# Performance work log

Measured on AMD Instinct MI355X. Metric: run time of the kernel, lower is better.

The kernel has to match this reference:

```python
import jax, jax.numpy as jnp
import numpy as np

B, N, C = 8, 1024, 768
H = 12
HD = C // H
R = 16  # LoRA rank
SCALE = HD ** -0.5


def setup_inputs() -> dict:
    key = jax.random.key(0)
    ks = jax.random.split(key, 13)
    s = C ** -0.5
    return {
        "x": jax.random.normal(ks[0], (B, N, C), jnp.float32),
        "Wq": jax.random.normal(ks[1], (C, C), jnp.float32) * s,
        "Wk": jax.random.normal(ks[2], (C, C), jnp.float32) * s,
        "Wv": jax.random.normal(ks[3], (C, C), jnp.float32) * s,
        "Wp": jax.random.normal(ks[4], (C, C), jnp.float32) * s,
        "bp": jax.random.normal(ks[5], (C,), jnp.float32) * 0.02,
        "la_q": jax.random.normal(ks[6], (C, R), jnp.float32) * s,
        "lb_q": jax.random.normal(ks[7], (R, C), jnp.float32) * (R ** -0.5),
        "la_k": jax.random.normal(ks[8], (C, R), jnp.float32) * s,
        "lb_k": jax.random.normal(ks[9], (R, C), jnp.float32) * (R ** -0.5),
        "la_v": jax.random.normal(ks[10], (C, R), jnp.float32) * s,
        "lb_v": jax.random.normal(ks[11], (R, C), jnp.float32) * (R ** -0.5),
        "block_weight": jax.random.uniform(ks[12], (3,), jnp.float32),
    }


def _split_heads(t):
    # [B, N, C] -> [B, H, N, HD]
    return t.reshape(B, N, H, HD).transpose(0, 2, 1, 3)


def reference(x, Wq, Wk, Wv, Wp, bp, la_q, lb_q, la_k, lb_k, la_v, lb_v, block_weight):
    # q/k/v projections (qkv_bias=False) + LoRA adapter injection (msa=[1,1,1])
    q = x @ Wq + block_weight[0] * ((x @ la_q) @ lb_q)
    k = x @ Wk + block_weight[1] * ((x @ la_k) @ lb_k)
    v = x @ Wv + block_weight[2] * ((x @ la_v) @ lb_v)

    qh = _split_heads(q)  # [B,H,N,HD]
    kh = _split_heads(k)
    vh = _split_heads(v)

    # full NxN scores, scale, softmax (attn_drop=0 -> identity)
    attn = jnp.einsum("bhnd,bhmd->bhnm", qh, kh) * SCALE
    attn = jax.nn.softmax(attn, axis=-1)
    out = jnp.einsum("bhnm,bhmd->bhnd", attn, vh)  # [B,H,N,HD]
    out = out.transpose(0, 2, 1, 3).reshape(B, N, C)

    # output projection (proj_drop=0 -> identity)
    return out @ Wp + bp
```

## Files before the change

### kernel.cpp

```cpp
#include <hip/hip_runtime.h>

#define BB 8
#define NN 1024
#define CC 768
#define HH 12
#define HD 64
#define RR 16
#define MM (BB * NN)
#define WSZ (CC * CC)
#define NT (NN / 64)

#define KSC 0.18033688011112042f

typedef short bf16x8 __attribute__((ext_vector_type(8)));
typedef short bf16x4 __attribute__((ext_vector_type(4)));
typedef float f32x4 __attribute__((ext_vector_type(4)));

__device__ __forceinline__ unsigned short f2bf(float f) {
    unsigned u = __builtin_bit_cast(unsigned, f);
    unsigned r = (u + 0x7FFFu + ((u >> 16) & 1u)) >> 16;
    return (unsigned short)r;
}
__device__ __forceinline__ float bf2f(unsigned short s) {
    return __builtin_bit_cast(float, ((unsigned)s) << 16);
}

__device__ __forceinline__ float fast_exp2(float x) {
#if __has_builtin(__builtin_amdgcn_exp2f)
    return __builtin_amdgcn_exp2f(x);
#else
    return exp2f(x);
#endif
}

__device__ __forceinline__ unsigned cvt_pk_bf16(float a, float b) {
    unsigned r;
    asm("v_cvt_pk_bf16_f32 %0, %1, %2" : "=v"(r) : "v"(a), "v"(b));
    return r;
}

__device__ __forceinline__ void gload16(const void* g, void* l) {
    __builtin_amdgcn_global_load_lds(
        (const __attribute__((address_space(1))) unsigned int*)g,
        (__attribute__((address_space(3))) unsigned int*)l, 16, 0, 0);
}

__global__ __launch_bounds__(256) void prep_w(
    const float* __restrict__ Wq, const float* __restrict__ Wk,
    const float* __restrict__ Wv, const float* __restrict__ Wp,
    const float* __restrict__ la_q, const float* __restrict__ lb_q,
    const float* __restrict__ la_k, const float* __restrict__ lb_k,
    const float* __restrict__ la_v, const float* __restrict__ lb_v,
    const float* __restrict__ bw, short* __restrict__ wt_hi,
    short* __restrict__ wt_lo) {
    __shared__ float laS[64][16];
    __shared__ float lbS[16][64];
    __shared__ float T[64][65];

    const int z = blockIdx.z;
    const int k0 = blockIdx.y * 64, n0 = blockIdx.x * 64;
    const int tid = threadIdx.x;

    const float* W = (z == 0) ? Wq : (z == 1) ? Wk : (z == 2) ? Wv : Wp;
    const float* la = (z == 0) ? la_q : (z == 1) ? la_k : la_v;
    const float* lb = (z == 0) ? lb_q : (z == 1) ? lb_k : lb_v;
    const float bwz = (z < 3) ? bw[z] : 0.f;

    if (z < 3) {
        #pragma unroll
        for (int e = 0; e < 4; ++e) {
            int idx = tid + 256 * e;
            laS[idx >> 4][idx & 15] = la[(size_t)(k0 + (idx >> 4)) * RR + (idx & 15)];
            lbS[idx >> 6][idx & 63] = lb[(size_t)(idx >> 6) * CC + n0 + (idx & 63)];
        }
    }
    __syncthreads();

    #pragma unroll
    for (int e = 0; e < 16; ++e) {
        int idx = tid + 256 * e;
        int row = idx >> 6, col = idx & 63;
        float v = W[(size_t)(k0 + row) * CC + n0 + col];
        if (z < 3) {
            float s = 0.f;
            #pragma unroll
            for (int r = 0; r < 16; ++r) s += laS[row][r] * lbS[r][col];
            v += bwz * s;
        }
        T[row][col] = v;
    }
    __syncthreads();

    short* oh = wt_hi + (size_t)z * WSZ;
    short* ol = wt_lo + (size_t)z * WSZ;
    #pragma unroll
    for (int e = 0; e < 16; ++e) {
        int idx = tid + 256 * e;
        int nrow = idx >> 6, kcol = idx & 63;
        float v = T[kcol][nrow];
        unsigned short hi = f2bf(v);
        unsigned short lo = f2bf(v - bf2f(hi));
        size_t off = (size_t)(n0 + nrow) * CC + k0 + kcol;
        oh[off] = (short)hi;
        ol[off] = (short)lo;
    }
}

__global__ __launch_bounds__(256) void prep_cvt(const float* __restrict__ src,
                                                short* __restrict__ hi, int n4) {
    int i = blockIdx.x * 256 + threadIdx.x;
    const int stride = gridDim.x * 256;
    for (; i < n4; i += stride) {
        f32x4 v = ((const f32x4*)src)[i];
        bf16x4 h;
        #pragma unroll
        for (int c = 0; c < 4; ++c) h[c] = (short)f2bf(v[c]);
        ((bf16x4*)hi)[i] = h;
    }
}

__device__ __forceinline__ void stage_plain(const short* __restrict__ gA,
                                            const short* __restrict__ gB,
                                            int rowA0, int rowB0, int kt,
                                            short* Lb, int tid) {
    const int fr = ((tid >> 6) << 4) | (tid & 15);
    const int kc = ((tid >> 4) & 3) * 8 + kt;
    const size_t ga0 = (size_t)(rowA0 + fr) * CC + kc;
    const size_t gb0 = (size_t)(rowB0 + fr) * CC + kc;
    short* d0 = Lb + tid * 8;
    short* d1 = Lb + (tid + 256) * 8;
    gload16(gA + ga0, d0);
    gload16(gA + ga0 + (size_t)64 * CC, d1);
    gload16(gB + gb0, d0 + 4096);
    gload16(gB + gb0 + (size_t)64 * CC, d1 + 4096);
}

__device__ __forceinline__ void gemm_core_plain(const short* __restrict__ gA,
                                                int rowA0,
                                                const short* __restrict__ gB,
                                                int rowB0, short (*L)[8192],
                                                f32x4 acc[4][4]) {
    const int tid = threadIdx.x, lane = tid & 63, w = tid >> 6;
    const int wm = w >> 1, wn = w & 1;
    stage_plain(gA, gB, rowA0, rowB0, 0, L[0], tid);
    __syncthreads();
    for (int ki = 0; ki < 24; ++ki) {
        if (ki < 23)
            stage_plain(gA, gB, rowA0, rowB0, (ki + 1) * 32, L[(ki + 1) & 1],
                        tid);
        const short* Lb = L[ki & 1];
        bf16x8 ah[4], bh[4];
        #pragma unroll
        for (int i = 0; i < 4; ++i)
            ah[i] = *(const bf16x8*)(Lb + (wm * 4 + i) * 512 + lane * 8);
        #pragma unroll
        for (int j = 0; j < 4; ++j)
            bh[j] = *(const bf16x8*)(Lb + 4096 + (wn * 4 + j) * 512 + lane * 8);
        #pragma unroll
        for (int i = 0; i < 4; ++i)
            #pragma unroll
            for (int j = 0; j < 4; ++j)
                acc[i][j] = __builtin_amdgcn_mfma_f32_16x16x32_bf16(
                    ah[i], bh[j], acc[i][j], 0, 0, 0);
        __syncthreads();
    }
}

__global__ __launch_bounds__(256, 4) void gemm_qkv(
    const short* __restrict__ xh, const short* __restrict__ wth,
    short* __restrict__ qb, short* __restrict__ kb, short* __restrict__ vtb) {
    __shared__ __align__(16) short L[2][8192];

    int flat = blockIdx.x + 6 * blockIdx.y + 384 * blockIdx.z;
    int swz = (flat & 7) * 144 + (flat >> 3);
    int z = swz / 384;
    int rem = swz - z * 384;
    int by = rem / 6, bx = rem - by * 6;
    const int m0 = by * 128, c0 = bx * 128;

    const short* wzh = wth + (size_t)z * WSZ;

    f32x4 acc[4][4];
    const f32x4 z4 = {0.f, 0.f, 0.f, 0.f};
    #pragma unroll
    for (int i = 0; i < 4; ++i)
        #pragma unroll
        for (int j = 0; j < 4; ++j) acc[i][j] = z4;

    const int lane = threadIdx.x & 63, w = threadIdx.x >> 6;
    const int wm = w >> 1, wn = w & 1, p = lane & 15, g = lane >> 4;

    if (z < 2) {
        gemm_core_plain(xh, m0, wzh, c0, L, acc);
        short* dst = (z == 0) ? qb : kb;
        const float scl = (z == 0) ? KSC : 1.0f;
        #pragma unroll
        for (int i = 0; i < 4; ++i) {
            #pragma unroll
            for (int r = 0; r < 4; ++r) {
                int m = m0 + wm * 64 + i * 16 + 4 * g + r;
                int b = m >> 10, n = m & 1023;
                #pragma unroll
                for (int j = 0; j < 4; ++j) {
                    int c = c0 + wn * 64 + j * 16 + p;
                    int h = c >> 6, d = c & 63;
                    dst[(((size_t)(b * HH + h)) * NN + n) * HD + d] =
                        (short)f2bf(acc[i][j][r] * scl);
                }
            }
        }
    } else {
        gemm_core_plain(wzh, c0, xh, m0, L, acc);
        #pragma unroll
        for (int i = 0; i < 4; ++i) {
            #pragma unroll
            for (int r = 0; r < 4; ++r) {
                int c = c0 + wm * 64 + i * 16 + 4 * g + r;
                int h = c >> 6, d = c & 63;
                #pragma unroll
                for (int j = 0; j < 4; ++j) {
                    int m = m0 + wn * 64 + j * 16 + p;
                    int b = m >> 10, n = m & 1023;
                    vtb[(((size_t)(b * HH + h)) * HD + d) * NN + n] =
                        (short)f2bf(acc[i][j][r]);
                }
            }
        }
    }
}

__device__ __forceinline__ void stage_kv(const short* __restrict__ kp,
                                         const short* __restrict__ vp, int j0,
                                         short* Kd, short* Vd, int tid) {
    const int pp = tid & 15;
    const int kc = ((tid >> 4) & 3) * 8 + ((tid >> 6) & 1) * 32;
    const int r0 = tid >> 7;
    gload16(kp + (size_t)(j0 + r0 * 16 + pp) * HD + kc, Kd + tid * 8);
    gload16(kp + (size_t)(j0 + (r0 + 2) * 16 + pp) * HD + kc, Kd + (tid + 256) * 8);
    gload16(vp + (size_t)(r0 * 16 + pp) * NN + j0 + kc, Vd + tid * 8);
    gload16(vp + (size_t)((r0 + 2) * 16 + pp) * NN + j0 + kc, Vd + (tid + 256) * 8);
}

__global__ __launch_bounds__(256, 4) void attn(const short* __restrict__ qb,
                                               const short* __restrict__ kb,
                                               const short* __restrict__ vtb,
                                               short* __restrict__ aoh,
                                               short* __restrict__ aol) {
    __shared__ __align__(16) short QP[4096];
    __shared__ __align__(16) short Kb[2][4096];
    __shared__ __align__(16) short Vb[2][4096];

    int flat = blockIdx.x + 16 * blockIdx.y;
    int swz = (flat & 7) * 192 + (flat >> 3);
    const int q0 = (swz & 15) * 64;
    const int bh = swz >> 4;

    const int tid = threadIdx.x, lane = tid & 63, w = tid >> 6;
    const int p = lane & 15, g = lane >> 4;
    const short* qp = qb + (size_t)bh * NN * HD;
    const short* kp = kb + (size_t)bh * NN * HD;
    const short* vp = vtb + (size_t)bh * NN * HD;

    {
        const int kc = ((tid >> 4) & 3) * 8 + ((tid >> 6) & 1) * 32;
        const int r0 = tid >> 7;
        gload16(qp + (size_t)(q0 + r0 * 16 + p) * HD + kc, QP + tid * 8);
        gload16(qp + (size_t)(q0 + (r0 + 2) * 16 + p) * HD + kc,
                QP + (tid + 256) * 8);
    }
    stage_kv(kp, vp, 0, Kb[0], Vb[0], tid);
    __syncthreads();

    bf16x8 bQ[2];
    bQ[0] = *(const bf16x8*)(QP + (w * 2 + 0) * 512 + lane * 8);
    bQ[1] = *(const bf16x8*)(QP + (w * 2 + 1) * 512 + lane * 8);

    float m_run = -1e30f, l_run = 0.f;
    f32x4 oacc[4];
    const f32x4 z4 = {0.f, 0.f, 0.f, 0.f};
    #pragma unroll
    for (int df = 0; df < 4; ++df) oacc[df] = z4;
    short* Pw = QP + w * 1024;

    for (int t = 0; t < NT; ++t) {
        if (t < NT - 1)
            stage_kv(kp, vp, (t + 1) * 64, Kb[(t + 1) & 1], Vb[(t + 1) & 1], tid);
        const short* Kc = Kb[t & 1];
        const short* Vc = Vb[t & 1];

        f32x4 sacc[4];
        #pragma unroll
        for (int jf = 0; jf < 4; ++jf) sacc[jf] = z4;
        #pragma unroll
        for (int ks = 0; ks < 2; ++ks) {
            #pragma unroll
            for (int jf = 0; jf < 4; ++jf) {
                bf16x8 aK =
                    *(const bf16x8*)(Kc + jf * 1024 + ks * 512 + lane * 8);
                sacc[jf] = __builtin_amdgcn_mfma_f32_16x16x32_bf16(
                    aK, bQ[ks], sacc[jf], 0, 0, 0);
            }
        }

        float tmax = sacc[0][0];
        #pragma unroll
        for (int jf = 0; jf < 4; ++jf)
            #pragma unroll
            for (int r = 0; r < 4; ++r) tmax = fmaxf(tmax, sacc[jf][r]);
        tmax = fmaxf(tmax, __shfl_xor(tmax, 16));
        tmax = fmaxf(tmax, __shfl_xor(tmax, 32));
        if (__any(tmax > m_run + 3.0f)) {
            const float mnew = fmaxf(m_run, tmax);
            const float fac = fast_exp2(m_run - mnew);
            m_run = mnew;
            l_run *= fac;
            #pragma unroll
            for (int r = 0; r < 4; ++r) {
                float fr = __shfl(fac, 4 * g + r, 16);
                #pragma unroll
                for (int df = 0; df < 4; ++df) oacc[df][r] *= fr;
            }
        }
        float lsum = 0.f;
        #pragma unroll
        for (int jf = 0; jf < 4; ++jf) {
            #pragma unroll
            for (int r = 0; r < 4; ++r) {
                float e = fast_exp2(sacc[jf][r] - m_run);
                sacc[jf][r] = e;
                lsum += e;
            }
        }
        lsum += __shfl_xor(lsum, 16);
        lsum += __shfl_xor(lsum, 32);
        l_run += lsum;

        #pragma unroll
        for (int jf = 0; jf < 4; ++jf) {
            uint2 wpk;
            wpk.x = cvt_pk_bf16(sacc[jf][0], sacc[jf][1]);
            wpk.y = cvt_pk_bf16(sacc[jf][2], sacc[jf][3]);
            *(uint2*)(Pw + (jf >> 1) * 512 +
                      (((jf & 1) * 2 + (g >> 1)) * 16 + p) * 8 + (g & 1) * 4) =
                wpk;
        }
        asm volatile("s_waitcnt lgkmcnt(0)" ::: "memory");
        __builtin_amdgcn_sched_barrier(0);

        #pragma unroll
        for (int ks = 0; ks < 2; ++ks) {
            bf16x8 aP = *(const bf16x8*)(Pw + ks * 512 + lane * 8);
            #pragma unroll
            for (int df = 0; df < 4; ++df) {
                bf16x8 bV =
                    *(const bf16x8*)(Vc + df * 1024 + ks * 512 + lane * 8);
                oacc[df] = __builtin_amdgcn_mfma_f32_16x16x32_bf16(
                    aP, bV, oacc[df], 0, 0, 0);
            }
        }
        __syncthreads();
    }

    const float inv = 1.f / l_run;
    const int b = bh / HH, h = bh % HH;
    #pragma unroll
    for (int r = 0; r < 4; ++r) {
        float ir = __shfl(inv, 4 * g + r, 16);
        int n = q0 + w * 16 + 4 * g + r;
        #pragma unroll
        for (int df = 0; df < 4; ++df) {
            float v = oacc[df][r] * ir;
            unsigned short hi = f2bf(v);
            unsigned short lo = f2bf(v - bf2f(hi));
            size_t off = ((size_t)(b * NN + n)) * CC + h * HD + df * 16 + p;
            aoh[off] = (short)hi;
            aol[off] = (short)lo;
        }
    }
}

__device__ __forceinline__ void stage_split(const short* __restrict__ gAh,
                                            const short* __restrict__ gAl,
                                            const short* __restrict__ gBh,
                                            const short* __restrict__ gBl,
                                            int rowA0, int rowB0, int kt,
                                            short* Lb, int tid) {
    const int fr = ((tid >> 6) << 4) | (tid & 15);
    const int kc = ((tid >> 4) & 3) * 8 + kt;
    const size_t ga0 = (size_t)(rowA0 + fr) * CC + kc;
    const size_t ga1 = ga0 + (size_t)64 * CC;
    const size_t gb0 = (size_t)(rowB0 + fr) * CC + kc;
    const size_t gb1 = gb0 + (size_t)64 * CC;
    short* d0 = Lb + tid * 8;
    short* d1 = Lb + (tid + 256) * 8;
    gload16(gAh + ga0, d0);
    gload16(gAh + ga1, d1);
    gload16(gAl + ga0, d0 + 4096);
    gload16(gAl + ga1, d1 + 4096);
    gload16(gBh + gb0, d0 + 8192);
    gload16(gBh + gb1, d1 + 8192);
    gload16(gBl + gb0, d0 + 12288);
    gload16(gBl + gb1, d1 + 12288);
}

__global__ __launch_bounds__(256, 3) void gemm_proj(
    const short* __restrict__ aoh, const short* __restrict__ aol,
    const short* __restrict__ wth, const short* __restrict__ wtl,
    const float* __restrict__ bp, float* __restrict__ out) {
    __shared__ __align__(16) short L[4 * 4096];

    int flat = blockIdx.x + 6 * blockIdx.y;
    int swz = (flat & 7) * 48 + (flat >> 3);
    int by = swz / 6, bx = swz - by * 6;
    const int m0 = by * 128, c0 = bx * 128;

    const short* wph = wth + (size_t)3 * WSZ;
    const short* wpl = wtl + (size_t)3 * WSZ;

    f32x4 acc[4][4];
    const f32x4 z4 = {0.f, 0.f, 0.f, 0.f};
    #pragma unroll
    for (int i = 0; i < 4; ++i)
        #pragma unroll
        for (int j = 0; j < 4; ++j) acc[i][j] = z4;

    const int tid = threadIdx.x, lane = tid & 63, w = tid >> 6;
    const int wm = w >> 1, wn = w & 1, p = lane & 15, g = lane >> 4;

    for (int kt = 0; kt < CC; kt += 32) {
        if (kt) __syncthreads();
        stage_split(aoh, aol, wph, wpl, m0, c0, kt, L, tid);
        __syncthreads();
        const int fb = lane * 8;
        bf16x8 ah[4], al[4], bh[4], bl[4];
        #pragma unroll
        for (int i = 0; i < 4; ++i) {
            ah[i] = *(const bf16x8*)(L + (wm * 4 + i) * 512 + fb);
            al[i] = *(const bf16x8*)(L + 4096 + (wm * 4 + i) * 512 + fb);
        }
        #pragma unroll
        for (int j = 0; j < 4; ++j) {
            bh[j] = *(const bf16x8*)(L + 8192 + (wn * 4 + j) * 512 + fb);
            bl[j] = *(const bf16x8*)(L + 12288 + (wn * 4 + j) * 512 + fb);
        }
        #pragma unroll
        for (int i = 0; i < 4; ++i) {
            #pragma unroll
            for (int j = 0; j < 4; ++j) {
                acc[i][j] = __builtin_amdgcn_mfma_f32_16x16x32_bf16(
                    ah[i], bh[j], acc[i][j], 0, 0, 0);
                acc[i][j] = __builtin_amdgcn_mfma_f32_16x16x32_bf16(
                    ah[i], bl[j], acc[i][j], 0, 0, 0);
                acc[i][j] = __builtin_amdgcn_mfma_f32_16x16x32_bf16(
                    al[i], bh[j], acc[i][j], 0, 0, 0);
            }
        }
    }

    float bpv[4];
    #pragma unroll
    for (int j = 0; j < 4; ++j) bpv[j] = bp[c0 + wn * 64 + j * 16 + p];

    #pragma unroll
    for (int i = 0; i < 4; ++i) {
        #pragma unroll
        for (int r = 0; r < 4; ++r) {
            int m = m0 + wm * 64 + i * 16 + 4 * g + r;
            #pragma unroll
            for (int j = 0; j < 4; ++j) {
                int c = c0 + wn * 64 + j * 16 + p;
                out[(size_t)m * CC + c] = acc[i][j][r] + bpv[j];
            }
        }
    }
}

extern "C" void kernel_launch(void* const* d_in, const int* in_sizes, int n_in,
                              void* d_out, int out_size, void* d_ws,
                              size_t ws_size, hipStream_t stream) {
    const float* x = (const float*)d_in[0];
    const float* Wq = (const float*)d_in[1];
    const float* Wk = (const float*)d_in[2];
    const float* Wv = (const float*)d_in[3];
    const float* Wp = (const float*)d_in[4];
    const float* bp = (const float*)d_in[5];
    const float* la_q = (const float*)d_in[6];
    const float* lb_q = (const float*)d_in[7];
    const float* la_k = (const float*)d_in[8];
    const float* lb_k = (const float*)d_in[9];
    const float* la_v = (const float*)d_in[10];
    const float* lb_v = (const float*)d_in[11];
    const float* bw = (const float*)d_in[12];
    float* out = (float*)d_out;

    short* ws = (short*)d_ws;
    short* wt_hi = ws;
    short* wt_lo = wt_hi + (size_t)4 * WSZ;
    short* x_hi = wt_lo + (size_t)4 * WSZ;
    short* qbuf = x_hi + (size_t)MM * CC;
    short* kbuf = qbuf + (size_t)MM * CC;
    short* vtbuf = kbuf + (size_t)MM * CC;
    short* aoh = vtbuf + (size_t)MM * CC;
    short* aol = aoh + (size_t)MM * CC;

    prep_w<<<dim3(CC / 64, CC / 64, 4), 256, 0, stream>>>(
        Wq, Wk, Wv, Wp, la_q, lb_q, la_k, lb_k, la_v, lb_v, bw, wt_hi, wt_lo);
    prep_cvt<<<2048, 256, 0, stream>>>(x, x_hi, MM * CC / 4);
    gemm_qkv<<<dim3(CC / 128, MM / 128, 3), 256, 0, stream>>>(
        x_hi, wt_hi, qbuf, kbuf, vtbuf);
    attn<<<dim3(NN / 64, BB * HH), 256, 0, stream>>>(qbuf, kbuf, vtbuf, aoh, aol);
    gemm_proj<<<dim3(CC / 128, MM / 128), 256, 0, stream>>>(aoh, aol, wt_hi,
                                                            wt_lo, bp, out);
}
```

Baseline: 273.1 us.

## Use single waitcnt+barrier per iteration and double-buffer proj GEMM staging

Replaces the two __syncthreads per loop iteration in the QKV GEMM core and attention loop with one explicit s_waitcnt vmcnt(0) plus s_barrier at the top of each iteration, so the async global-to-LDS loads are waited on explicitly. The output projection GEMM moves from a single LDS buffer with load-then-compute to a double-buffered prefetch pipeline. Launch bounds change (qkv to 5 blocks/SM, proj to 2 because of the doubled LDS). Dropping the trailing barrier relies on the next iteration's barrier to protect buffer reuse, and proj occupancy falls.

After: 349.0 us. +27.8%, slower.

```diff
diff --git a/kernel.cpp b/kernel.cpp
--- a/kernel.cpp
+++ b/kernel.cpp
@@ -43,6 +43,11 @@
     __builtin_amdgcn_global_load_lds(
         (const __attribute__((address_space(1))) unsigned int*)g,
         (__attribute__((address_space(3))) unsigned int*)l, 16, 0, 0);
+}
+
+__device__ __forceinline__ void wait_vm0_barrier() {
+    asm volatile("s_waitcnt vmcnt(0)" ::: "memory");
+    __builtin_amdgcn_s_barrier();
 }
 
 __global__ __launch_bounds__(256) void prep_w(
@@ -143,8 +148,8 @@
     const int tid = threadIdx.x, lane = tid & 63, w = tid >> 6;
     const int wm = w >> 1, wn = w & 1;
     stage_plain(gA, gB, rowA0, rowB0, 0, L[0], tid);
-    __syncthreads();
     for (int ki = 0; ki < 24; ++ki) {
+        wait_vm0_barrier();
         if (ki < 23)
             stage_plain(gA, gB, rowA0, rowB0, (ki + 1) * 32, L[(ki + 1) & 1],
                         tid);
@@ -162,11 +167,10 @@
             for (int j = 0; j < 4; ++j)
                 acc[i][j] = __builtin_amdgcn_mfma_f32_16x16x32_bf16(
                     ah[i], bh[j], acc[i][j], 0, 0, 0);
-        __syncthreads();
-    }
-}
-
-__global__ __launch_bounds__(256, 4) void gemm_qkv(
+    }
+}
+
+__global__ __launch_bounds__(256, 5) void gemm_qkv(
     const short* __restrict__ xh, const short* __restrict__ wth,
     short* __restrict__ qb, short* __restrict__ kb, short* __restrict__ vtb) {
     __shared__ __align__(16) short L[2][8192];
@@ -269,7 +273,7 @@
                 QP + (tid + 256) * 8);
     }
     stage_kv(kp, vp, 0, Kb[0], Vb[0], tid);
-    __syncthreads();
+    wait_vm0_barrier();
 
     bf16x8 bQ[2];
     bQ[0] = *(const bf16x8*)(QP + (w * 2 + 0) * 512 + lane * 8);
@@ -283,6 +287,7 @@
     short* Pw = QP + w * 1024;
 
     for (int t = 0; t < NT; ++t) {
+        if (t) wait_vm0_barrier();
         if (t < NT - 1)
             stage_kv(kp, vp, (t + 1) * 64, Kb[(t + 1) & 1], Vb[(t + 1) & 1], tid);
         const short* Kc = Kb[t & 1];
@@ -358,7 +363,6 @@
                     aP, bV, oacc[df], 0, 0, 0);
             }
         }
-        __syncthreads();
     }
 
     const float inv = 1.f / l_run;
@@ -403,11 +407,11 @@
     gload16(gBl + gb1, d1 + 12288);
 }
 
-__global__ __launch_bounds__(256, 3) void gemm_proj(
+__global__ __launch_bounds__(256, 2) void gemm_proj(
     const short* __restrict__ aoh, const short* __restrict__ aol,
     const short* __restrict__ wth, const short* __restrict__ wtl,
     const float* __restrict__ bp, float* __restrict__ out) {
-    __shared__ __align__(16) short L[4 * 4096];
+    __shared__ __align__(16) short L[2][4 * 4096];
 
     int flat = blockIdx.x + 6 * blockIdx.y;
     int swz = (flat & 7) * 48 + (flat >> 3);
@@ -427,21 +431,24 @@
     const int tid = threadIdx.x, lane = tid & 63, w = tid >> 6;
     const int wm = w >> 1, wn = w & 1, p = lane & 15, g = lane >> 4;
 
-    for (int kt = 0; kt < CC; kt += 32) {
-        if (kt) __syncthreads();
-        stage_split(aoh, aol, wph, wpl, m0, c0, kt, L, tid);
-        __syncthreads();
+    stage_split(aoh, aol, wph, wpl, m0, c0, 0, L[0], tid);
+    for (int ki = 0; ki < 24; ++ki) {
+        wait_vm0_barrier();
+        if (ki < 23)
+            stage_split(aoh, aol, wph, wpl, m0, c0, (ki + 1) * 32,
+                        L[(ki + 1) & 1], tid);
+        const short* Lb = L[ki & 1];
         const int fb = lane * 8;
         bf16x8 ah[4], al[4], bh[4], bl[4];
         #pragma unroll
         for (int i = 0; i < 4; ++i) {
-            ah[i] = *(const bf16x8*)(L + (wm * 4 + i) * 512 + fb);
-            al[i] = *(const bf16x8*)(L + 4096 + (wm * 4 + i) * 512 + fb);
+            ah[i] = *(const bf16x8*)(Lb + (wm * 4 + i) * 512 + fb);
+            al[i] = *(const bf16x8*)(Lb + 4096 + (wm * 4 + i) * 512 + fb);
         }
         #pragma unroll
         for (int j = 0; j < 4; ++j) {
-            bh[j] = *(const bf16x8*)(L + 8192 + (wn * 4 + j) * 512 + fb);
-            bl[j] = *(const bf16x8*)(L + 12288 + (wn * 4 + j) * 512 + fb);
+            bh[j] = *(const bf16x8*)(Lb + 8192 + (wn * 4 + j) * 512 + fb);
+            bl[j] = *(const bf16x8*)(Lb + 12288 + (wn * 4 + j) * 512 + fb);
         }
         #pragma unroll
         for (int i = 0; i < 4; ++i) {
```
